# Kernel tuning notes

Hardware: AMD Instinct MI355X
Metric: run time of the kernel (lower is better)

Reference implementation:

```python
import jax, jax.numpy as jnp
import numpy as np

P = 16         # patch size
D = 192        # embed dim (vit_tiny)
NH = 3         # heads
DEPTH = 12
HID = 768      # mlp hidden = 4*D
NCLS = 1000
PCT = 0.25
EPS = 1e-6


def _ln(x, s, b):
    m = x.mean(-1, keepdims=True)
    v = ((x - m) ** 2).mean(-1, keepdims=True)
    return (x - m) * jax.lax.rsqrt(v + EPS) * s + b


def setup_inputs() -> dict:
    key = jax.random.key(0)
    ks = jax.random.split(key, 24)
    B, IMG = 64, 384
    std = 0.02
    d = {
        "magno_image": jax.random.normal(ks[0], (B, 3, IMG, IMG), jnp.float32),
        "line_drawing": jax.random.uniform(ks[1], (B, 1, IMG, IMG), jnp.float32),
        "conv_w": jax.random.normal(ks[2], (D, 3, P, P), jnp.float32) * std,
        "conv_b": jnp.zeros((D,), jnp.float32),
        "pos_embed": jax.random.normal(ks[3], (1, (IMG // P) ** 2 + 1, D), jnp.float32) * std,
        "cls_token": jax.random.normal(ks[4], (1, 1, D), jnp.float32) * std,
        "ln1_s": jnp.ones((DEPTH, D), jnp.float32),
        "ln1_b": jnp.zeros((DEPTH, D), jnp.float32),
        "qkv_w": jax.random.normal(ks[5], (DEPTH, D, 3 * D), jnp.float32) * std,
        "qkv_b": jnp.zeros((DEPTH, 3 * D), jnp.float32),
        "proj_w": jax.random.normal(ks[6], (DEPTH, D, D), jnp.float32) * std,
        "proj_b": jnp.zeros((DEPTH, D), jnp.float32),
        "ln2_s": jnp.ones((DEPTH, D), jnp.float32),
        "ln2_b": jnp.zeros((DEPTH, D), jnp.float32),
        "fc1_w": jax.random.normal(ks[7], (DEPTH, D, HID), jnp.float32) * std,
        "fc1_b": jnp.zeros((DEPTH, HID), jnp.float32),
        "fc2_w": jax.random.normal(ks[8], (DEPTH, HID, D), jnp.float32) * std,
        "fc2_b": jnp.zeros((DEPTH, D), jnp.float32),
        "normf_s": jnp.ones((D,), jnp.float32),
        "normf_b": jnp.zeros((D,), jnp.float32),
        "head_w": jax.random.normal(ks[9], (D, NCLS), jnp.float32) * std,
        "head_b": jnp.zeros((NCLS,), jnp.float32),
    }
    return d


def _forward(magno_image, line_drawing, conv_w, conv_b, pos_embed, cls_token,
             ln1_s, ln1_b, qkv_w, qkv_b, proj_w, proj_b, ln2_s, ln2_b,
             fc1_w, fc1_b, fc2_w, fc2_b, normf_s, normf_b, head_w, head_b):
    B, _, IMG, _ = magno_image.shape
    g = IMG // P
    N = g * g
    k = int(N * PCT)
    hd = D // NH

    # --- PatchImportanceScorer: avg-pool(patch_size) then flatten ---
    scores = line_drawing.reshape(B, g, P, g, P).mean(axis=(2, 4)).reshape(B, N)

    # --- patch embed (conv stride == kernel == reshaped matmul) ---
    x = magno_image.reshape(B, 3, g, P, g, P).transpose(0, 2, 4, 1, 3, 5)
    patches = x.reshape(B, N, 3 * P * P) @ conv_w.reshape(D, 3 * P * P).T + conv_b

    # --- top_k selection + gather of patches and pos-embed ---
    _, idx = jax.lax.top_k(scores, k)                      # (B, k)
    sel = jnp.take_along_axis(patches, idx[:, :, None], axis=1)
    pos = jnp.take_along_axis(
        jnp.broadcast_to(pos_embed[:, 1:, :], (B, N, D)), idx[:, :, None], axis=1)
    sel = sel + pos

    cls = jnp.broadcast_to(cls_token + pos_embed[:, :1, :], (B, 1, D))
    seq = jnp.concatenate([cls, sel], axis=1)              # (B, 1+k, D)
    S = 1 + k

    def block(h, p):
        l1s, l1b, qw, qb, pw, pb, l2s, l2b, f1w, f1b, f2w, f2b = p
        y = _ln(h, l1s, l1b)
        qkv = (y @ qw + qb).reshape(B, S, 3, NH, hd)
        q, kk, v = qkv[:, :, 0], qkv[:, :, 1], qkv[:, :, 2]  # (B,S,NH,hd)
        att = jnp.einsum('bqhd,bkhd->bhqk', q, kk) / np.sqrt(hd).astype(np.float32)
        att = jax.nn.softmax(att, axis=-1)
        o = jnp.einsum('bhqk,bkhd->bqhd', att, v).reshape(B, S, D)
        h = h + o @ pw + pb
        y = _ln(h, l2s, l2b)
        h = h + jax.nn.gelu(y @ f1w + f1b, approximate=False) @ f2w + f2b
        return h, None

    seq, _ = jax.lax.scan(block, seq, (ln1_s, ln1_b, qkv_w, qkv_b, proj_w, proj_b,
                                       ln2_s, ln2_b, fc1_w, fc1_b, fc2_w, fc2_b))
    seq = _ln(seq, normf_s, normf_b)
    return seq[:, 0] @ head_w + head_b


def reference(magno_image, line_drawing, conv_w, conv_b, pos_embed, cls_token,
              ln1_s, ln1_b, qkv_w, qkv_b, proj_w, proj_b, ln2_s, ln2_b,
              fc1_w, fc1_b, fc2_w, fc2_b, normf_s, normf_b, head_w, head_b):
    return _forward(magno_image, line_drawing, conv_w, conv_b, pos_embed, cls_token,
                    ln1_s, ln1_b, qkv_w, qkv_b, proj_w, proj_b, ln2_s, ln2_b,
                    fc1_w, fc1_b, fc2_w, fc2_b, normf_s, normf_b, head_w, head_b)
```

## Files before the change

kernel.cpp:

```cpp
#include <hip/hip_runtime.h>
#include <hip/hip_bf16.h>
#include <cmath>


#define Bsz   64
#define NPATCH 576
#define KSEL  144
#define SEQ   145
#define DIM   192
#define HIDN  768

typedef __bf16 bf16x8 __attribute__((ext_vector_type(8)));
typedef float  f32x4  __attribute__((ext_vector_type(4)));

__global__ __launch_bounds__(256) void scores_kernel(const float* __restrict__ line,
                                                     float* __restrict__ scores)
{
    int gp = blockIdx.x;
    int b = gp / NPATCH, p = gp % NPATCH;
    int gy = p / 24, gx = p % 24;
    int t = threadIdx.x, py = t >> 4, px = t & 15;
    float v = line[((size_t)b * 384 + gy * 16 + py) * 384 + gx * 16 + px];
    for (int off = 32; off; off >>= 1) v += __shfl_xor(v, off);
    __shared__ float red[4];
    if ((t & 63) == 0) red[t >> 6] = v;
    __syncthreads();
    if (t == 0) scores[gp] = (red[0] + red[1] + red[2] + red[3]) * (1.f / 256.f);
}

__global__ __launch_bounds__(256) void topk_kernel(const float* __restrict__ scores,
                                                   int* __restrict__ idx)
{
    int b = blockIdx.x;
    __shared__ float s[NPATCH];
    for (int i = threadIdx.x; i < NPATCH; i += 256) s[i] = scores[b * NPATCH + i];
    __syncthreads();
    for (int i = threadIdx.x; i < NPATCH; i += 256) {
        float si = s[i];
        int cnt = 0;
        for (int j = 0; j < NPATCH; ++j) {
            float sj = s[j];
            cnt += (sj > si) || (sj == si && j < i);
        }
        if (cnt < KSEL) idx[b * KSEL + cnt] = i;
    }
}

__global__ __launch_bounds__(256) void gather_kernel(const float* __restrict__ magno,
                                                     const int* __restrict__ idx,
                                                     __hip_bfloat16* __restrict__ selp)
{
    int bs = blockIdx.x;
    int b = bs / KSEL;
    int pi = idx[bs];
    int gy = pi / 24, gx = pi % 24;
    int t = threadIdx.x, py = t >> 4, px = t & 15;
    size_t src = ((size_t)b * 3 * 384 + gy * 16 + py) * 384 + gx * 16 + px;
    __hip_bfloat16* dst = &selp[(size_t)bs * 768];
#pragma unroll
    for (int c = 0; c < 3; ++c)
        dst[c * 256 + t] = __float2bfloat16(magno[src + (size_t)c * 384 * 384]);
}

__global__ __launch_bounds__(256) void convert_bf16_kernel(const float* __restrict__ src,
                                                           __hip_bfloat16* __restrict__ dst,
                                                           int n)
{
    int i = blockIdx.x * 256 + threadIdx.x;
    if (i < n) dst[i] = __float2bfloat16(src[i]);
}

__global__ __launch_bounds__(256) void transpose_w_kernel(const float* __restrict__ src,
                                                          __hip_bfloat16* __restrict__ dst,
                                                          int R, int C)
{
    __shared__ float t[32][33];
    size_t lo = (size_t)blockIdx.z * R * C;
    int r0 = blockIdx.y * 32, c0 = blockIdx.x * 32;
    int tx = threadIdx.x & 31, ty = threadIdx.x >> 5;
#pragma unroll
    for (int i = 0; i < 32; i += 8)
        t[ty + i][tx] = src[lo + (size_t)(r0 + ty + i) * C + c0 + tx];
    __syncthreads();
#pragma unroll
    for (int i = 0; i < 32; i += 8)
        dst[lo + (size_t)(c0 + ty + i) * R + r0 + tx] = __float2bfloat16(t[tx][ty + i]);
}

__global__ void cls_kernel(const float* __restrict__ cls, const float* __restrict__ pos,
                           float* __restrict__ h)
{
    int b = blockIdx.x, t = threadIdx.x;
    h[(size_t)b * SEQ * DIM + t] = cls[t] + pos[t];
}

__global__ __launch_bounds__(256) void ln_kernel(const float* __restrict__ x,
                                                 const float* __restrict__ s,
                                                 const float* __restrict__ bia,
                                                 __hip_bfloat16* __restrict__ y, int ntok)
{
    int w = threadIdx.x >> 6, lane = threadIdx.x & 63;
    int tok = blockIdx.x * 4 + w;
    if (tok >= ntok) return;
    const float* xp = &x[(size_t)tok * DIM];
    float x0 = xp[lane], x1 = xp[lane + 64], x2 = xp[lane + 128];
    float sum = x0 + x1 + x2;
    for (int off = 32; off; off >>= 1) sum += __shfl_xor(sum, off);
    float mean = sum * (1.f / 192.f);
    float d0 = x0 - mean, d1 = x1 - mean, d2 = x2 - mean;
    float vs = d0 * d0 + d1 * d1 + d2 * d2;
    for (int off = 32; off; off >>= 1) vs += __shfl_xor(vs, off);
    float rs = rsqrtf(vs * (1.f / 192.f) + 1e-6f);
    __hip_bfloat16* yp = &y[(size_t)tok * DIM];
    yp[lane]       = __float2bfloat16(d0 * rs * s[lane]       + bia[lane]);
    yp[lane + 64]  = __float2bfloat16(d1 * rs * s[lane + 64]  + bia[lane + 64]);
    yp[lane + 128] = __float2bfloat16(d2 * rs * s[lane + 128] + bia[lane + 128]);
}

template <int MODE>
__global__ __launch_bounds__(256) void gemm_bf16(const __hip_bfloat16* __restrict__ A,
                                                 const __hip_bfloat16* __restrict__ Wt,
                                                 const float* __restrict__ bias,
                                                 void* __restrict__ Cout,
                                                 int M, int N, int K,
                                                 const int* __restrict__ selidx,
                                                 const float* __restrict__ pos)
{
    __shared__ __align__(16) char As[8192];
    __shared__ __align__(16) char Bs[8192];
    const int tid = threadIdx.x;
    const int lane = tid & 63, wid = tid >> 6;
    const int wr = wid >> 1, wc = wid & 1;
    const int lr = lane & 15, lk = lane >> 4;
    const int m0 = blockIdx.y * 64, n0 = blockIdx.x * 64;
    f32x4 acc[2][2] = {};

    for (int k0 = 0; k0 < K; k0 += 64) {
#pragma unroll
        for (int it = 0; it < 2; ++it) {
            int chunk = it * 256 + tid;
            int r = chunk >> 3, g = chunk & 7;
            int loff = r * 128 + ((g ^ (r & 7)) * 16);
            *reinterpret_cast<uint4*>(As + loff) =
                *reinterpret_cast<const uint4*>(&A[(size_t)(m0 + r) * K + k0 + g * 8]);
            *reinterpret_cast<uint4*>(Bs + loff) =
                *reinterpret_cast<const uint4*>(&Wt[(size_t)(n0 + r) * K + k0 + g * 8]);
        }
        __syncthreads();
#pragma unroll
        for (int kc = 0; kc < 2; ++kc) {
            int g = kc * 4 + lk;
            bf16x8 af[2], bfr[2];
#pragma unroll
            for (int mi = 0; mi < 2; ++mi) {
                int r = wr * 32 + mi * 16 + lr;
                af[mi] = *reinterpret_cast<const bf16x8*>(As + r * 128 + ((g ^ (r & 7)) * 16));
            }
#pragma unroll
            for (int ni = 0; ni < 2; ++ni) {
                int r = wc * 32 + ni * 16 + lr;
                bfr[ni] = *reinterpret_cast<const bf16x8*>(Bs + r * 128 + ((g ^ (r & 7)) * 16));
            }
#pragma unroll
            for (int mi = 0; mi < 2; ++mi)
#pragma unroll
                for (int ni = 0; ni < 2; ++ni)
                    acc[mi][ni] = __builtin_amdgcn_mfma_f32_16x16x32_bf16(
                        af[mi], bfr[ni], acc[mi][ni], 0, 0, 0);
        }
        __syncthreads();
    }

#pragma unroll
    for (int mi = 0; mi < 2; ++mi)
#pragma unroll
    for (int ni = 0; ni < 2; ++ni)
#pragma unroll
    for (int j = 0; j < 4; ++j) {
        int row = m0 + wr * 32 + mi * 16 + (lane >> 4) * 4 + j;
        int col = n0 + wc * 32 + ni * 16 + (lane & 15);
        float v = acc[mi][ni][j] + bias[col];
        if (MODE == 2) {
            ((__hip_bfloat16*)Cout)[(size_t)row * N + col] =
                __float2bfloat16(0.5f * v * (1.f + erff(v * 0.70710678118654752f)));
        } else {
            int bb2 = row / KSEL, ss = row % KSEL;
            int pi = selidx[row];
            v += pos[(size_t)(1 + pi) * DIM + col];
            ((float*)Cout)[((size_t)bb2 * SEQ + 1 + ss) * DIM + col] = v;
        }
    }
}

__global__ __launch_bounds__(256) void gemm_qkv(const __hip_bfloat16* __restrict__ A,
                                                const __hip_bfloat16* __restrict__ Wt,
                                                const float* __restrict__ bias,
                                                __hip_bfloat16* __restrict__ qk,
                                                __hip_bfloat16* __restrict__ Vt)
{
    __shared__ __align__(16) char As[8192];
    __shared__ __align__(16) char Bs[8192];
    const int tid = threadIdx.x;
    const int lane = tid & 63, wid = tid >> 6;
    const int wr = wid >> 1, wc = wid & 1;
    const int lr = lane & 15, lk = lane >> 4;
    const int m0 = blockIdx.y * 64, n0 = blockIdx.x * 64;
    const int K = DIM;
    f32x4 acc[2][2] = {};

    for (int k0 = 0; k0 < K; k0 += 64) {
#pragma unroll
        for (int it = 0; it < 2; ++it) {
            int chunk = it * 256 + tid;
            int r = chunk >> 3, g = chunk & 7;
            int loff = r * 128 + ((g ^ (r & 7)) * 16);
            *reinterpret_cast<uint4*>(As + loff) =
                *reinterpret_cast<const uint4*>(&A[(size_t)(m0 + r) * K + k0 + g * 8]);
            *reinterpret_cast<uint4*>(Bs + loff) =
                *reinterpret_cast<const uint4*>(&Wt[(size_t)(n0 + r) * K + k0 + g * 8]);
        }
        __syncthreads();
#pragma unroll
        for (int kc = 0; kc < 2; ++kc) {
            int g = kc * 4 + lk;
            bf16x8 af[2], bfr[2];
#pragma unroll
            for (int mi = 0; mi < 2; ++mi) {
                int r = wr * 32 + mi * 16 + lr;
                af[mi] = *reinterpret_cast<const bf16x8*>(As + r * 128 + ((g ^ (r & 7)) * 16));
            }
#pragma unroll
            for (int ni = 0; ni < 2; ++ni) {
                int r = wc * 32 + ni * 16 + lr;
                bfr[ni] = *reinterpret_cast<const bf16x8*>(Bs + r * 128 + ((g ^ (r & 7)) * 16));
            }
#pragma unroll
            for (int mi = 0; mi < 2; ++mi)
#pragma unroll
                for (int ni = 0; ni < 2; ++ni)
                    acc[mi][ni] = __builtin_amdgcn_mfma_f32_16x16x32_bf16(
                        af[mi], bfr[ni], acc[mi][ni], 0, 0, 0);
        }
        __syncthreads();
    }

#pragma unroll
    for (int mi = 0; mi < 2; ++mi)
#pragma unroll
    for (int ni = 0; ni < 2; ++ni)
#pragma unroll
    for (int j = 0; j < 4; ++j) {
        int row = m0 + wr * 32 + mi * 16 + (lane >> 4) * 4 + j;
        int col = n0 + wc * 32 + ni * 16 + (lane & 15);
        float v = acc[mi][ni][j] + bias[col];
        if (col < 384) {
            qk[(size_t)row * 384 + col] = __float2bfloat16(v);
        } else {
            int c = col - 384;
            int b = row / SEQ, s = row - b * SEQ;
            Vt[((size_t)(b * 3 + (c >> 6)) * 64 + (c & 63)) * 160 + s] = __float2bfloat16(v);
        }
    }
}

__global__ __launch_bounds__(256) void attnproj_kernel(const __hip_bfloat16* __restrict__ qk,
                                                       const __hip_bfloat16* __restrict__ Vt,
                                                       const __hip_bfloat16* __restrict__ Wp,
                                                       const float* __restrict__ pbias,
                                                       float* __restrict__ h,
                                                       const float* __restrict__ ls,
                                                       const float* __restrict__ lb,
                                                       __hip_bfloat16* __restrict__ y)
{
    const int b = blockIdx.y, qt = blockIdx.x;
    const int tid = threadIdx.x;
    const int w = tid >> 6, lane = tid & 63;
    const int lr = lane & 15, lg = lane >> 4;
    __shared__ __hip_bfloat16 Ps[3][32][168];
    __shared__ __hip_bfloat16 Ot[32][200];
    __shared__ float redsum[4][32];
    __shared__ float redsq[4][32];

    const size_t qbase = (size_t)b * SEQ * 384;
    const int q0 = qt * 32;

    if (w < 3) {
        const int hh = w;
        bf16x8 aq[2][2];
#pragma unroll
        for (int mi = 0; mi < 2; ++mi)
#pragma unroll
            for (int ks = 0; ks < 2; ++ks)
                aq[mi][ks] = *reinterpret_cast<const bf16x8*>(
                    &qk[qbase + (size_t)(q0 + mi * 16 + lr) * 384 + hh * 64 + ks * 32 + lg * 8]);
        f32x4 sc[2][10];
#pragma unroll
        for (int mi = 0; mi < 2; ++mi)
#pragma unroll
            for (int nf = 0; nf < 10; ++nf) sc[mi][nf] = (f32x4){0.f, 0.f, 0.f, 0.f};
#pragma unroll
        for (int nf = 0; nf < 10; ++nf) {
            int key = nf * 16 + lr;
#pragma unroll
            for (int ks = 0; ks < 2; ++ks) {
                bf16x8 bk = *reinterpret_cast<const bf16x8*>(
                    &qk[qbase + (size_t)key * 384 + 192 + hh * 64 + ks * 32 + lg * 8]);
#pragma unroll
                for (int mi = 0; mi < 2; ++mi)
                    sc[mi][nf] = __builtin_amdgcn_mfma_f32_16x16x32_bf16(
                        aq[mi][ks], bk, sc[mi][nf], 0, 0, 0);
            }
        }
#pragma unroll
        for (int mi = 0; mi < 2; ++mi) {
            float mx[4] = {-1e30f, -1e30f, -1e30f, -1e30f};
#pragma unroll
            for (int nf = 0; nf < 10; ++nf) {
                bool valid = nf * 16 + lr < SEQ;
#pragma unroll
                for (int j = 0; j < 4; ++j) {
                    float v = valid ? sc[mi][nf][j] * 0.125f : -1e30f;
                    sc[mi][nf][j] = v;
                    mx[j] = fmaxf(mx[j], v);
                }
            }
#pragma unroll
            for (int j = 0; j < 4; ++j)
                for (int off = 1; off < 16; off <<= 1)
                    mx[j] = fmaxf(mx[j], __shfl_xor(mx[j], off));
            float sm[4] = {0.f, 0.f, 0.f, 0.f};
#pragma unroll
            for (int nf = 0; nf < 10; ++nf)
#pragma unroll
                for (int j = 0; j < 4; ++j) {
                    float p = __expf(sc[mi][nf][j] - mx[j]);
                    sc[mi][nf][j] = p;
                    sm[j] += p;
                }
#pragma unroll
            for (int j = 0; j < 4; ++j) {
                for (int off = 1; off < 16; off <<= 1) sm[j] += __shfl_xor(sm[j], off);
                sm[j] = 1.f / sm[j];
            }
#pragma unroll
            for (int nf = 0; nf < 10; ++nf) {
                int key = nf * 16 + lr;
#pragma unroll
                for (int j = 0; j < 4; ++j)
                    Ps[hh][mi * 16 + lg * 4 + j][key] = __float2bfloat16(sc[mi][nf][j] * sm[j]);
            }
        }
        const __hip_bfloat16* vtb = &Vt[(size_t)(b * 3 + hh) * 64 * 160];
        f32x4 oacc[2][4];
#pragma unroll
        for (int mi = 0; mi < 2; ++mi)
#pragma unroll
            for (int nf = 0; nf < 4; ++nf) oacc[mi][nf] = (f32x4){0.f, 0.f, 0.f, 0.f};
#pragma unroll
        for (int ks = 0; ks < 5; ++ks) {
            bf16x8 ap[2];
            ap[0] = *reinterpret_cast<const bf16x8*>(&Ps[hh][lr][ks * 32 + lg * 8]);
            ap[1] = *reinterpret_cast<const bf16x8*>(&Ps[hh][16 + lr][ks * 32 + lg * 8]);
#pragma unroll
            for (int nf = 0; nf < 4; ++nf) {
                bf16x8 bv = *reinterpret_cast<const bf16x8*>(
                    &vtb[(size_t)(nf * 16 + lr) * 160 + ks * 32 + lg * 8]);
#pragma unroll
                for (int mi = 0; mi < 2; ++mi)
                    oacc[mi][nf] = __builtin_amdgcn_mfma_f32_16x16x32_bf16(
                        ap[mi], bv, oacc[mi][nf], 0, 0, 0);
            }
        }
#pragma unroll
        for (int mi = 0; mi < 2; ++mi)
#pragma unroll
            for (int nf = 0; nf < 4; ++nf)
#pragma unroll
                for (int j = 0; j < 4; ++j)
                    Ot[mi * 16 + lg * 4 + j][hh * 64 + nf * 16 + lr] =
                        __float2bfloat16(oacc[mi][nf][j]);
    }
    __syncthreads();

    f32x4 pacc[2][3];
#pragma unroll
    for (int mi = 0; mi < 2; ++mi)
#pragma unroll
        for (int nf = 0; nf < 3; ++nf) pacc[mi][nf] = (f32x4){0.f, 0.f, 0.f, 0.f};
#pragma unroll
    for (int kk = 0; kk < 6; ++kk) {
        bf16x8 af[2];
        af[0] = *reinterpret_cast<const bf16x8*>(&Ot[lr][kk * 32 + lg * 8]);
        af[1] = *reinterpret_cast<const bf16x8*>(&Ot[16 + lr][kk * 32 + lg * 8]);
#pragma unroll
        for (int nf = 0; nf < 3; ++nf) {
            int ncol = w * 48 + nf * 16 + lr;
            bf16x8 bw = *reinterpret_cast<const bf16x8*>(&Wp[(size_t)ncol * 192 + kk * 32 + lg * 8]);
#pragma unroll
            for (int mi = 0; mi < 2; ++mi)
                pacc[mi][nf] = __builtin_amdgcn_mfma_f32_16x16x32_bf16(
                    af[mi], bw, pacc[mi][nf], 0, 0, 0);
        }
    }
    float v[2][3][4];
    float psum[2][4] = {}, psq[2][4] = {};
#pragma unroll
    for (int mi = 0; mi < 2; ++mi)
#pragma unroll
    for (int nf = 0; nf < 3; ++nf) {
        int col = w * 48 + nf * 16 + lr;
        float bcol = pbias[col];
#pragma unroll
        for (int j = 0; j < 4; ++j) {
            int q = q0 + mi * 16 + lg * 4 + j;
            float res = (q < SEQ) ? h[((size_t)b * SEQ + q) * DIM + col] : 0.f;
            float t = pacc[mi][nf][j] + bcol + res;
            v[mi][nf][j] = t;
            psum[mi][j] += t;
            psq[mi][j] += t * t;
        }
    }
#pragma unroll
    for (int mi = 0; mi < 2; ++mi)
#pragma unroll
        for (int j = 0; j < 4; ++j) {
            for (int off = 1; off < 16; off <<= 1) {
                psum[mi][j] += __shfl_xor(psum[mi][j], off);
                psq[mi][j]  += __shfl_xor(psq[mi][j], off);
            }
            redsum[w][mi * 16 + lg * 4 + j] = psum[mi][j];
            redsq[w][mi * 16 + lg * 4 + j]  = psq[mi][j];
        }
    __syncthreads();
#pragma unroll
    for (int mi = 0; mi < 2; ++mi) {
#pragma unroll
        for (int j = 0; j < 4; ++j) {
            int r = mi * 16 + lg * 4 + j;
            int q = q0 + r;
            if (q >= SEQ) continue;
            float tsum = redsum[0][r] + redsum[1][r] + redsum[2][r] + redsum[3][r];
            float tsq  = redsq[0][r]  + redsq[1][r]  + redsq[2][r]  + redsq[3][r];
            float mean = tsum * (1.f / 192.f);
            float var  = tsq * (1.f / 192.f) - mean * mean;
            float rs = rsqrtf(var + 1e-6f);
#pragma unroll
            for (int nf = 0; nf < 3; ++nf) {
                int col = w * 48 + nf * 16 + lr;
                float t = v[mi][nf][j];
                h[((size_t)b * SEQ + q) * DIM + col] = t;
                y[((size_t)b * SEQ + q) * DIM + col] =
                    __float2bfloat16((t - mean) * rs * ls[col] + lb[col]);
            }
        }
    }
}

template <bool DO_LN>
__global__ __launch_bounds__(256) void gemm_res_ln(const __hip_bfloat16* __restrict__ A,
                                                   const __hip_bfloat16* __restrict__ Wt,
                                                   const float* __restrict__ bias,
                                                   float* __restrict__ h,
                                                   const float* __restrict__ ls,
                                                   const float* __restrict__ lb,
                                                   __hip_bfloat16* __restrict__ y,
                                                   int K)
{
    __shared__ __align__(16) char As[8192];
    __shared__ __align__(16) char Bs[24576];
    const int tid = threadIdx.x;
    const int lane = tid & 63, w = tid >> 6;
    const int lr = lane & 15, lg = lane >> 4;
    const int m0 = blockIdx.x * 64;
    f32x4 acc[12] = {};

    for (int k0 = 0; k0 < K; k0 += 64) {
        {
            int chunk = tid;
#pragma unroll
            for (int it = 0; it < 2; ++it, chunk += 256) {
                int r = chunk >> 3, g = chunk & 7;
                *reinterpret_cast<uint4*>(As + r * 128 + ((g ^ (r & 7)) * 16)) =
                    *reinterpret_cast<const uint4*>(&A[(size_t)(m0 + r) * K + k0 + g * 8]);
            }
        }
        {
            int chunk = tid;
#pragma unroll
            for (int it = 0; it < 6; ++it, chunk += 256) {
                int r = chunk >> 3, g = chunk & 7;
                *reinterpret_cast<uint4*>(Bs + r * 128 + ((g ^ (r & 7)) * 16)) =
                    *reinterpret_cast<const uint4*>(&Wt[(size_t)r * K + k0 + g * 8]);
            }
        }
        __syncthreads();
#pragma unroll
        for (int kc = 0; kc < 2; ++kc) {
            int g = kc * 4 + lg;
            int ar = w * 16 + lr;
            bf16x8 af = *reinterpret_cast<const bf16x8*>(As + ar * 128 + ((g ^ (ar & 7)) * 16));
#pragma unroll
            for (int nf = 0; nf < 12; ++nf) {
                int br = nf * 16 + lr;
                bf16x8 bfv = *reinterpret_cast<const bf16x8*>(Bs + br * 128 + ((g ^ (br & 7)) * 16));
                acc[nf] = __builtin_amdgcn_mfma_f32_16x16x32_bf16(af, bfv, acc[nf], 0, 0, 0);
            }
        }
        __syncthreads();
    }

    float v[12][4];
    float sum[4] = {0.f, 0.f, 0.f, 0.f};
#pragma unroll
    for (int nf = 0; nf < 12; ++nf) {
        int col = nf * 16 + lr;
#pragma unroll
        for (int j = 0; j < 4; ++j) {
            int row = m0 + w * 16 + lg * 4 + j;
            float t = acc[nf][j] + bias[col] + h[(size_t)row * DIM + col];
            v[nf][j] = t;
            h[(size_t)row * DIM + col] = t;
            sum[j] += t;
        }
    }
    if (DO_LN) {
#pragma unroll
        for (int j = 0; j < 4; ++j)
            for (int off = 1; off < 16; off <<= 1) sum[j] += __shfl_xor(sum[j], off);
        float mean[4], sq[4] = {0.f, 0.f, 0.f, 0.f};
#pragma unroll
        for (int j = 0; j < 4; ++j) mean[j] = sum[j] * (1.f / 192.f);
#pragma unroll
        for (int nf = 0; nf < 12; ++nf)
#pragma unroll
            for (int j = 0; j < 4; ++j) {
                float d = v[nf][j] - mean[j];
                sq[j] += d * d;
            }
#pragma unroll
        for (int j = 0; j < 4; ++j) {
            for (int off = 1; off < 16; off <<= 1) sq[j] += __shfl_xor(sq[j], off);
            sq[j] = rsqrtf(sq[j] * (1.f / 192.f) + 1e-6f);
        }
#pragma unroll
        for (int nf = 0; nf < 12; ++nf) {
            int col = nf * 16 + lr;
            float sc = ls[col], bc = lb[col];
#pragma unroll
            for (int j = 0; j < 4; ++j) {
                int row = m0 + w * 16 + lg * 4 + j;
                y[(size_t)row * DIM + col] =
                    __float2bfloat16((v[nf][j] - mean[j]) * sq[j] * sc + bc);
            }
        }
    }
}

__global__ __launch_bounds__(256) void head_kernel(const float* __restrict__ h,
                                                   const float* __restrict__ nfs,
                                                   const float* __restrict__ nfb,
                                                   const float* __restrict__ hw,
                                                   const float* __restrict__ hb,
                                                   float* __restrict__ out)
{
    int b = blockIdx.x, t = threadIdx.x;
    __shared__ float y[DIM];
    __shared__ float red[4];
    float x = (t < DIM) ? h[(size_t)b * SEQ * DIM + t] : 0.f;
    float sum = x;
    for (int off = 32; off; off >>= 1) sum += __shfl_xor(sum, off);
    if ((t & 63) == 0) red[t >> 6] = sum;
    __syncthreads();
    float mean = (red[0] + red[1] + red[2] + red[3]) * (1.f / 192.f);
    __syncthreads();
    float d = (t < DIM) ? (x - mean) : 0.f;
    float v = d * d;
    for (int off = 32; off; off >>= 1) v += __shfl_xor(v, off);
    if ((t & 63) == 0) red[t >> 6] = v;
    __syncthreads();
    float var = (red[0] + red[1] + red[2] + red[3]) * (1.f / 192.f);
    float rs = rsqrtf(var + 1e-6f);
    if (t < DIM) y[t] = d * rs * nfs[t] + nfb[t];
    __syncthreads();
    for (int n = t; n < 1000; n += 256) {
        float acc = hb[n];
#pragma unroll 8
        for (int k = 0; k < DIM; ++k)
            acc = fmaf(y[k], hw[(size_t)k * 1000 + n], acc);
        out[(size_t)b * 1000 + n] = acc;
    }
}

extern "C" void kernel_launch(void* const* d_in, const int* in_sizes, int n_in,
                              void* d_out, int out_size, void* d_ws, size_t ws_size,
                              hipStream_t stream)
{
    const float* magno  = (const float*)d_in[0];
    const float* line   = (const float*)d_in[1];
    const float* conv_w = (const float*)d_in[2];
    const float* conv_b = (const float*)d_in[3];
    const float* pos    = (const float*)d_in[4];
    const float* cls    = (const float*)d_in[5];
    const float* ln1_s  = (const float*)d_in[6];
    const float* ln1_b  = (const float*)d_in[7];
    const float* qkv_w  = (const float*)d_in[8];
    const float* qkv_b  = (const float*)d_in[9];
    const float* proj_w = (const float*)d_in[10];
    const float* proj_b = (const float*)d_in[11];
    const float* ln2_s  = (const float*)d_in[12];
    const float* ln2_b  = (const float*)d_in[13];
    const float* fc1_w  = (const float*)d_in[14];
    const float* fc1_b  = (const float*)d_in[15];
    const float* fc2_w  = (const float*)d_in[16];
    const float* fc2_b  = (const float*)d_in[17];
    const float* normf_s = (const float*)d_in[18];
    const float* normf_b = (const float*)d_in[19];
    const float* head_w = (const float*)d_in[20];
    const float* head_b = (const float*)d_in[21];
    float* out = (float*)d_out;
    (void)in_sizes; (void)n_in; (void)out_size; (void)ws_size;

    char* ws = (char*)d_ws;
    int*            idx     = (int*)            (ws + 0);
    float*          h       = (float*)          (ws + 147456);
    __hip_bfloat16* y       = (__hip_bfloat16*) (ws + 7274496);
    __hip_bfloat16* qk      = (__hip_bfloat16*) (ws + 10838016);
    __hip_bfloat16* Vt      = (__hip_bfloat16*) (ws + 17965056);
    __hip_bfloat16* tbuf    = (__hip_bfloat16*) (ws + 21897216);
    __hip_bfloat16* wt_qkv  = (__hip_bfloat16*) (ws + 36151296);
    __hip_bfloat16* wt_proj = (__hip_bfloat16*) (ws + 38805504);
    __hip_bfloat16* wt_fc1  = (__hip_bfloat16*) (ws + 39690240);
    __hip_bfloat16* wt_fc2  = (__hip_bfloat16*) (ws + 43229184);
    float*          scoresbuf = (float*)qk;
    __hip_bfloat16* convT     = y;
    __hip_bfloat16* selp      = tbuf;

    hipMemsetAsync(Vt, 0, 3932160, stream);
    transpose_w_kernel<<<dim3(18, 6, 12), 256, 0, stream>>>(qkv_w, wt_qkv, DIM, 576);
    transpose_w_kernel<<<dim3(6, 6, 12),  256, 0, stream>>>(proj_w, wt_proj, DIM, DIM);
    transpose_w_kernel<<<dim3(24, 6, 12), 256, 0, stream>>>(fc1_w, wt_fc1, DIM, HIDN);
    transpose_w_kernel<<<dim3(6, 24, 12), 256, 0, stream>>>(fc2_w, wt_fc2, HIDN, DIM);
    convert_bf16_kernel<<<576, 256, 0, stream>>>(conv_w, convT, DIM * 768);

    scores_kernel<<<Bsz * NPATCH, 256, 0, stream>>>(line, scoresbuf);
    topk_kernel<<<Bsz, 256, 0, stream>>>(scoresbuf, idx);
    gather_kernel<<<Bsz * KSEL, 256, 0, stream>>>(magno, idx, selp);
    cls_kernel<<<Bsz, DIM, 0, stream>>>(cls, pos, h);
    gemm_bf16<3><<<dim3(3, 144), 256, 0, stream>>>(selp, convT, conv_b, h,
                                                   9216, DIM, 768, idx, pos);

    const int ntok = Bsz * SEQ;
    ln_kernel<<<ntok / 4, 256, 0, stream>>>(h, ln1_s, ln1_b, y, ntok);
    for (int l = 0; l < 12; ++l) {
        gemm_qkv<<<dim3(9, 145), 256, 0, stream>>>(y, wt_qkv + (size_t)l * 576 * DIM,
                                                   qkv_b + l * 576, qk, Vt);
        attnproj_kernel<<<dim3(5, Bsz), 256, 0, stream>>>(qk, Vt,
                                                          wt_proj + (size_t)l * DIM * DIM,
                                                          proj_b + l * DIM, h,
                                                          ln2_s + l * DIM, ln2_b + l * DIM, y);
        gemm_bf16<2><<<dim3(12, 145), 256, 0, stream>>>(y, wt_fc1 + (size_t)l * HIDN * DIM,
                                                        fc1_b + l * HIDN, tbuf,
                                                        ntok, HIDN, DIM, nullptr, nullptr);
        if (l < 11)
            gemm_res_ln<true><<<145, 256, 0, stream>>>(tbuf, wt_fc2 + (size_t)l * DIM * HIDN,
                                                       fc2_b + l * DIM, h,
                                                       ln1_s + (l + 1) * DIM, ln1_b + (l + 1) * DIM,
                                                       y, HIDN);
        else
            gemm_res_ln<false><<<145, 256, 0, stream>>>(tbuf, wt_fc2 + (size_t)l * DIM * HIDN,
                                                        fc2_b + l * DIM, h,
                                                        nullptr, nullptr, y, HIDN);
    }
    head_kernel<<<Bsz, 256, 0, stream>>>(h, normf_s, normf_b, head_w, head_b, out);
}
```

Before: 940.8 us.

## Fuse fc1+GELU and fc2+residual+LayerNorm into one MLP kernel

Replaces the separate fc1 GEMM (GELU epilogue writing a bf16 hidden buffer to global memory) and the fc2 residual/LN GEMM with one kernel per 32-token tile. The 768-wide GELU activations stay in LDS, removing the global write and read of the hidden tensor and one launch per layer. fc2 now splits its 192 output columns across the four waves, with LayerNorm statistics combined through shared memory. Weights are read straight from global/L2 by every block instead of being staged in LDS, so L2 traffic grows. The large LDS footprint may also limit how many blocks fit per CU.

New measurement: 1.313 ms. 39.5% more time.

```diff
diff --git a/kernel.cpp b/kernel.cpp
--- a/kernel.cpp
+++ b/kernel.cpp
@@ -117,14 +117,13 @@
     yp[lane + 128] = __float2bfloat16(d2 * rs * s[lane + 128] + bia[lane + 128]);
 }
 
-template <int MODE>
-__global__ __launch_bounds__(256) void gemm_bf16(const __hip_bfloat16* __restrict__ A,
-                                                 const __hip_bfloat16* __restrict__ Wt,
-                                                 const float* __restrict__ bias,
-                                                 void* __restrict__ Cout,
-                                                 int M, int N, int K,
-                                                 const int* __restrict__ selidx,
-                                                 const float* __restrict__ pos)
+__global__ __launch_bounds__(256) void gemm_embed(const __hip_bfloat16* __restrict__ A,
+                                                  const __hip_bfloat16* __restrict__ Wt,
+                                                  const float* __restrict__ bias,
+                                                  float* __restrict__ h,
+                                                  int M, int N, int K,
+                                                  const int* __restrict__ selidx,
+                                                  const float* __restrict__ pos)
 {
     __shared__ __align__(16) char As[8192];
     __shared__ __align__(16) char Bs[8192];
@@ -180,15 +179,10 @@
         int row = m0 + wr * 32 + mi * 16 + (lane >> 4) * 4 + j;
         int col = n0 + wc * 32 + ni * 16 + (lane & 15);
         float v = acc[mi][ni][j] + bias[col];
-        if (MODE == 2) {
-            ((__hip_bfloat16*)Cout)[(size_t)row * N + col] =
-                __float2bfloat16(0.5f * v * (1.f + erff(v * 0.70710678118654752f)));
-        } else {
-            int bb2 = row / KSEL, ss = row % KSEL;
-            int pi = selidx[row];
-            v += pos[(size_t)(1 + pi) * DIM + col];
-            ((float*)Cout)[((size_t)bb2 * SEQ + 1 + ss) * DIM + col] = v;
-        }
+        int bb2 = row / KSEL, ss = row % KSEL;
+        int pi = selidx[row];
+        v += pos[(size_t)(1 + pi) * DIM + col];
+        h[((size_t)bb2 * SEQ + 1 + ss) * DIM + col] = v;
     }
 }
 
@@ -457,100 +451,155 @@
 }
 
 template <bool DO_LN>
-__global__ __launch_bounds__(256) void gemm_res_ln(const __hip_bfloat16* __restrict__ A,
-                                                   const __hip_bfloat16* __restrict__ Wt,
-                                                   const float* __restrict__ bias,
-                                                   float* __restrict__ h,
-                                                   const float* __restrict__ ls,
-                                                   const float* __restrict__ lb,
-                                                   __hip_bfloat16* __restrict__ y,
-                                                   int K)
-{
-    __shared__ __align__(16) char As[8192];
-    __shared__ __align__(16) char Bs[24576];
+__global__ __launch_bounds__(256) void mlp_kernel(const __hip_bfloat16* __restrict__ yin,
+                                                  const __hip_bfloat16* __restrict__ W1t,
+                                                  const float* __restrict__ b1,
+                                                  const __hip_bfloat16* __restrict__ W2t,
+                                                  const float* __restrict__ b2,
+                                                  float* __restrict__ h,
+                                                  const float* __restrict__ ls,
+                                                  const float* __restrict__ lb,
+                                                  __hip_bfloat16* __restrict__ yout)
+{
+    __shared__ __align__(16) char As[12288];
+    __shared__ __align__(16) char Ts[49152];
+    __shared__ float redsum[4][32];
+    __shared__ float redsq[4][32];
     const int tid = threadIdx.x;
     const int lane = tid & 63, w = tid >> 6;
     const int lr = lane & 15, lg = lane >> 4;
-    const int m0 = blockIdx.x * 64;
-    f32x4 acc[12] = {};
-
-    for (int k0 = 0; k0 < K; k0 += 64) {
-        {
-            int chunk = tid;
-#pragma unroll
-            for (int it = 0; it < 2; ++it, chunk += 256) {
-                int r = chunk >> 3, g = chunk & 7;
-                *reinterpret_cast<uint4*>(As + r * 128 + ((g ^ (r & 7)) * 16)) =
-                    *reinterpret_cast<const uint4*>(&A[(size_t)(m0 + r) * K + k0 + g * 8]);
-            }
-        }
-        {
-            int chunk = tid;
-#pragma unroll
-            for (int it = 0; it < 6; ++it, chunk += 256) {
-                int r = chunk >> 3, g = chunk & 7;
-                *reinterpret_cast<uint4*>(Bs + r * 128 + ((g ^ (r & 7)) * 16)) =
-                    *reinterpret_cast<const uint4*>(&Wt[(size_t)r * K + k0 + g * 8]);
-            }
-        }
+    const int m0 = blockIdx.x * 32;
+
+    for (int c = tid; c < 768; c += 256) {
+        int r = c / 24, g = c % 24;
+        *reinterpret_cast<uint4*>(As + r * 384 + ((g ^ (r & 7)) * 16)) =
+            *reinterpret_cast<const uint4*>(&yin[(size_t)(m0 + r) * DIM + g * 8]);
+    }
+    __syncthreads();
+
+    {
+        f32x4 acc[2][12] = {};
+#pragma unroll
+        for (int ks = 0; ks < 6; ++ks) {
+            int g = ks * 4 + lg;
+            bf16x8 af[2];
+#pragma unroll
+            for (int mi = 0; mi < 2; ++mi) {
+                int r = mi * 16 + lr;
+                af[mi] = *reinterpret_cast<const bf16x8*>(As + r * 384 + ((g ^ (r & 7)) * 16));
+            }
+#pragma unroll
+            for (int nf = 0; nf < 12; ++nf) {
+                int col = w * 192 + nf * 16 + lr;
+                bf16x8 bw = *reinterpret_cast<const bf16x8*>(
+                    &W1t[(size_t)col * DIM + ks * 32 + lg * 8]);
+#pragma unroll
+                for (int mi = 0; mi < 2; ++mi)
+                    acc[mi][nf] = __builtin_amdgcn_mfma_f32_16x16x32_bf16(
+                        af[mi], bw, acc[mi][nf], 0, 0, 0);
+            }
+        }
+#pragma unroll
+        for (int mi = 0; mi < 2; ++mi)
+#pragma unroll
+        for (int nf = 0; nf < 12; ++nf) {
+            int col = w * 192 + nf * 16 + lr;
+            float bcol = b1[col];
+            int g2 = col >> 3, sub = col & 7;
+#pragma unroll
+            for (int j = 0; j < 4; ++j) {
+                int r = mi * 16 + lg * 4 + j;
+                float vv = acc[mi][nf][j] + bcol;
+                float ge = 0.5f * vv * (1.f + erff(vv * 0.70710678118654752f));
+                *reinterpret_cast<__hip_bfloat16*>(
+                    Ts + r * 1536 + ((g2 ^ (r & 7)) * 16) + sub * 2) = __float2bfloat16(ge);
+            }
+        }
+    }
+    __syncthreads();
+
+    f32x4 pacc[2][3] = {};
+#pragma unroll
+    for (int ks = 0; ks < 24; ++ks) {
+        int g = ks * 4 + lg;
+        bf16x8 af[2];
+#pragma unroll
+        for (int mi = 0; mi < 2; ++mi) {
+            int r = mi * 16 + lr;
+            af[mi] = *reinterpret_cast<const bf16x8*>(Ts + r * 1536 + ((g ^ (r & 7)) * 16));
+        }
+#pragma unroll
+        for (int nf = 0; nf < 3; ++nf) {
+            int col = w * 48 + nf * 16 + lr;
+            bf16x8 bw = *reinterpret_cast<const bf16x8*>(
+                &W2t[(size_t)col * HIDN + ks * 32 + lg * 8]);
+#pragma unroll
+            for (int mi = 0; mi < 2; ++mi)
+                pacc[mi][nf] = __builtin_amdgcn_mfma_f32_16x16x32_bf16(
+                    af[mi], bw, pacc[mi][nf], 0, 0, 0);
+        }
+    }
+
+    float v[2][3][4];
+    float psum[2][4] = {}, psq[2][4] = {};
+#pragma unroll
+    for (int mi = 0; mi < 2; ++mi)
+#pragma unroll
+    for (int nf = 0; nf < 3; ++nf) {
+        int col = w * 48 + nf * 16 + lr;
+        float bcol = b2[col];
+#pragma unroll
+        for (int j = 0; j < 4; ++j) {
+            int row = m0 + mi * 16 + lg * 4 + j;
+            float t = pacc[mi][nf][j] + bcol + h[(size_t)row * DIM + col];
+            v[mi][nf][j] = t;
+            psum[mi][j] += t;
+            psq[mi][j] += t * t;
+        }
+    }
+    if (DO_LN) {
+#pragma unroll
+        for (int mi = 0; mi < 2; ++mi)
+#pragma unroll
+            for (int j = 0; j < 4; ++j) {
+                for (int off = 1; off < 16; off <<= 1) {
+                    psum[mi][j] += __shfl_xor(psum[mi][j], off);
+                    psq[mi][j]  += __shfl_xor(psq[mi][j], off);
+                }
+                redsum[w][mi * 16 + lg * 4 + j] = psum[mi][j];
+                redsq[w][mi * 16 + lg * 4 + j]  = psq[mi][j];
+            }
         __syncthreads();
 #pragma unroll
-        for (int kc = 0; kc < 2; ++kc) {
-            int g = kc * 4 + lg;
-            int ar = w * 16 + lr;
-            bf16x8 af = *reinterpret_cast<const bf16x8*>(As + ar * 128 + ((g ^ (ar & 7)) * 16));
-#pragma unroll
-            for (int nf = 0; nf < 12; ++nf) {
-                int br = nf * 16 + lr;
-                bf16x8 bfv = *reinterpret_cast<const bf16x8*>(Bs + br * 128 + ((g ^ (br & 7)) * 16));
-                acc[nf] = __builtin_amdgcn_mfma_f32_16x16x32_bf16(af, bfv, acc[nf], 0, 0, 0);
-            }
-        }
-        __syncthreads();
-    }
-
-    float v[12][4];
-    float sum[4] = {0.f, 0.f, 0.f, 0.f};
-#pragma unroll
-    for (int nf = 0; nf < 12; ++nf) {
-        int col = nf * 16 + lr;
-#pragma unroll
-        for (int j = 0; j < 4; ++j) {
-            int row = m0 + w * 16 + lg * 4 + j;
-            float t = acc[nf][j] + bias[col] + h[(size_t)row * DIM + col];
-            v[nf][j] = t;
-            h[(size_t)row * DIM + col] = t;
-            sum[j] += t;
-        }
-    }
-    if (DO_LN) {
-#pragma unroll
-        for (int j = 0; j < 4; ++j)
-            for (int off = 1; off < 16; off <<= 1) sum[j] += __shfl_xor(sum[j], off);
-        float mean[4], sq[4] = {0.f, 0.f, 0.f, 0.f};
-#pragma unroll
-        for (int j = 0; j < 4; ++j) mean[j] = sum[j] * (1.f / 192.f);
-#pragma unroll
-        for (int nf = 0; nf < 12; ++nf)
+        for (int mi = 0; mi < 2; ++mi)
 #pragma unroll
             for (int j = 0; j < 4; ++j) {
-                float d = v[nf][j] - mean[j];
-                sq[j] += d * d;
-            }
-#pragma unroll
-        for (int j = 0; j < 4; ++j) {
-            for (int off = 1; off < 16; off <<= 1) sq[j] += __shfl_xor(sq[j], off);
-            sq[j] = rsqrtf(sq[j] * (1.f / 192.f) + 1e-6f);
-        }
-#pragma unroll
-        for (int nf = 0; nf < 12; ++nf) {
-            int col = nf * 16 + lr;
-            float sc = ls[col], bc = lb[col];
+                int r = mi * 16 + lg * 4 + j;
+                int row = m0 + r;
+                float tsum = redsum[0][r] + redsum[1][r] + redsum[2][r] + redsum[3][r];
+                float tsq  = redsq[0][r]  + redsq[1][r]  + redsq[2][r]  + redsq[3][r];
+                float mean = tsum * (1.f / 192.f);
+                float var  = tsq * (1.f / 192.f) - mean * mean;
+                float rs = rsqrtf(var + 1e-6f);
+#pragma unroll
+                for (int nf = 0; nf < 3; ++nf) {
+                    int col = w * 48 + nf * 16 + lr;
+                    float t = v[mi][nf][j];
+                    h[(size_t)row * DIM + col] = t;
+                    yout[(size_t)row * DIM + col] =
+                        __float2bfloat16((t - mean) * rs * ls[col] + lb[col]);
+                }
+            }
+    } else {
+#pragma unroll
+        for (int mi = 0; mi < 2; ++mi)
+#pragma unroll
+        for (int nf = 0; nf < 3; ++nf) {
+            int col = w * 48 + nf * 16 + lr;
 #pragma unroll
             for (int j = 0; j < 4; ++j) {
-                int row = m0 + w * 16 + lg * 4 + j;
-                y[(size_t)row * DIM + col] =
-                    __float2bfloat16((v[nf][j] - mean[j]) * sq[j] * sc + bc);
+                int row = m0 + mi * 16 + lg * 4 + j;
+                h[(size_t)row * DIM + col] = v[mi][nf][j];
             }
         }
     }
@@ -646,8 +695,8 @@
     topk_kernel<<<Bsz, 256, 0, stream>>>(scoresbuf, idx);
     gather_kernel<<<Bsz * KSEL, 256, 0, stream>>>(magno, idx, selp);
     cls_kernel<<<Bsz, DIM, 0, stream>>>(cls, pos, h);
-    gemm_bf16<3><<<dim3(3, 144), 256, 0, stream>>>(selp, convT, conv_b, h,
-                                                   9216, DIM, 768, idx, pos);
+    gemm_embed<<<dim3(3, 144), 256, 0, stream>>>(selp, convT, conv_b, h,
+                                                 9216, DIM, 768, idx, pos);
 
     const int ntok = Bsz * SEQ;
     ln_kernel<<<ntok / 4, 256, 0, stream>>>(h, ln1_s, ln1_b, y, ntok);
@@ -658,18 +707,16 @@
                                                           wt_proj + (size_t)l * DIM * DIM,
                                                           proj_b + l * DIM, h,
                                                           ln2_s + l * DIM, ln2_b + l * DIM, y);
-        gemm_bf16<2><<<dim3(12, 145), 256, 0, stream>>>(y, wt_fc1 + (size_t)l * HIDN * DIM,
-                                                        fc1_b + l * HIDN, tbuf,
-                                                        ntok, HIDN, DIM, nullptr, nullptr);
         if (l < 11)
-            gemm_res_ln<true><<<145, 256, 0, stream>>>(tbuf, wt_fc2 + (size_t)l * DIM * HIDN,
-                                                       fc2_b + l * DIM, h,
-                                                       ln1_s + (l + 1) * DIM, ln1_b + (l + 1) * DIM,
-                                                       y, HIDN);
+            mlp_kernel<true><<<ntok / 32, 256, 0, stream>>>(
+                y, wt_fc1 + (size_t)l * HIDN * DIM, fc1_b + l * HIDN,
+                wt_fc2 + (size_t)l * DIM * HIDN, fc2_b + l * DIM, h,
+                ln1_s + (l + 1) * DIM, ln1_b + (l + 1) * DIM, y);
         else
-            gemm_res_ln<false><<<145, 256, 0, stream>>>(tbuf, wt_fc2 + (size_t)l * DIM * HIDN,
-                                                        fc2_b + l * DIM, h,
-                                                        nullptr, nullptr, y, HIDN);
+            mlp_kernel<false><<<ntok / 32, 256, 0, stream>>>(
+                y, wt_fc1 + (size_t)l * HIDN * DIM, fc1_b + l * HIDN,
+                wt_fc2 + (size_t)l * DIM * HIDN, fc2_b + l * DIM, h,
+                nullptr, nullptr, y);
     }
     head_kernel<<<Bsz, 256, 0, stream>>>(h, normf_s, normf_b, head_w, head_b, out);
 }
```
